# Kernel tuning notes

Hardware: AMD Instinct MI355X
Metric: run time of the kernel (lower is better)

The kernel has to match this reference:

```python
import jax, jax.numpy as jnp
import numpy as np

B, S, E = 2, 2048, 1024
H = 16
D = E // H
LAYER_IDX = 2.0
MASKED_BIAS = -10000.0


def setup_inputs() -> dict:
    key = jax.random.key(0)
    k1, k2, k3 = jax.random.split(key, 3)
    hidden_state = jax.random.normal(k1, (B, S, E), dtype=jnp.float32)
    w_attn = jax.random.normal(k2, (E, 3 * E), dtype=jnp.float32) * 0.2
    b_attn = jnp.zeros((3 * E,), dtype=jnp.float32)
    w_proj = jax.random.normal(k3, (E, E), dtype=jnp.float32) * 0.2
    b_proj = jnp.zeros((E,), dtype=jnp.float32)
    return {"hidden_state": hidden_state, "w_attn": w_attn, "b_attn": b_attn,
            "w_proj": w_proj, "b_proj": b_proj}


def reference(hidden_state, w_attn, b_attn, w_proj, b_proj):
    b, s, e = hidden_state.shape
    # c_attn: Conv1D == x @ W + b, then split into q, k, v
    qkv = hidden_state @ w_attn + b_attn          # [b, s, 3E]
    q, k, v = jnp.split(qkv, 3, axis=-1)
    # split heads -> [b, H, s, D]
    def split_heads(t):
        return t.reshape(b, s, H, D).transpose(0, 2, 1, 3)
    q, k, v = split_heads(q), split_heads(k), split_heads(v)
    # QK^T scaled by sqrt(d_head) then by layer_idx
    scores = jnp.einsum("bhqd,bhkd->bhqk", q, k)
    scores = scores / jnp.asarray(D ** 0.5, scores.dtype)
    scores = scores / LAYER_IDX
    # causal mask with masked_bias fill (-10000.0), matching bias buffer slice
    causal = jnp.tril(jnp.ones((s, s), dtype=bool))  # [s, s]
    scores = jnp.where(causal[None, None, :, :], scores, jnp.asarray(MASKED_BIAS, scores.dtype))
    attn = jax.nn.softmax(scores, axis=-1)
    out = jnp.einsum("bhqk,bhkd->bhqd", attn, v)   # [b, H, s, D]
    # merge heads
    out = out.transpose(0, 2, 1, 3).reshape(b, s, e)
    # c_proj
    return out @ w_proj + b_proj
```

## Files before the change

kernel.cpp:

```cpp
#include <hip/hip_runtime.h>
#include <cstddef>
#include <cstdint>

#define B_DIM   2
#define S_LEN   2048
#define EMB     1024
#define NH      16
#define HD      64
#define QKV_N   3072
#define MROWS   (B_DIM * S_LEN)

using half8  = __attribute__((ext_vector_type(8))) _Float16;
using half4  = __attribute__((ext_vector_type(4))) _Float16;
using f32x4  = __attribute__((ext_vector_type(4))) float;

#if defined(__has_builtin)
#if __has_builtin(__builtin_amdgcn_global_load_lds)
#define HAS_GLL 1
#endif
#endif

__device__ __forceinline__ void stage16(const _Float16* g, _Float16* lds_base, int lane)
{
#ifdef HAS_GLL
    (void)lane;
    __builtin_amdgcn_global_load_lds(
        (const __attribute__((address_space(1))) unsigned int*)g,
        (__attribute__((address_space(3))) unsigned int*)lds_base, 16, 0, 0);
#else
    *(half8*)(lds_base + lane * 8) = *(const half8*)g;
#endif
}

__global__ __launch_bounds__(256)
void prep_all(const float* __restrict__ hidden, const float* __restrict__ w_attn,
              const float* __restrict__ w_proj, _Float16* __restrict__ hidden_h,
              _Float16* __restrict__ wattn_t, _Float16* __restrict__ wproj_t)
{
    const int bid = blockIdx.x, t = threadIdx.x;
    if (bid < 4096) {
        int i = bid * 1024 + t * 4;
        float4 v = *(const float4*)(hidden + i);
        half4 h = { (_Float16)v.x, (_Float16)v.y, (_Float16)v.z, (_Float16)v.w };
        *(half4*)(hidden_h + i) = h;
        return;
    }
    __shared__ float T[32][33];
    const float* W; _Float16* Wt; int N, bx, by;
    if (bid < 7168) {
        int t2 = bid - 4096; bx = t2 % 96; by = t2 / 96; W = w_attn; Wt = wattn_t; N = QKV_N;
    } else {
        int t3 = bid - 7168; bx = t3 & 31; by = t3 >> 5; W = w_proj; Wt = wproj_t; N = EMB;
    }
    const int n0 = bx * 32, k0 = by * 32;
    const int r = t >> 3, c4 = (t & 7) * 4;
    float4 w = *(const float4*)(W + (size_t)(k0 + r) * N + n0 + c4);
    T[r][c4 + 0] = w.x; T[r][c4 + 1] = w.y;
    T[r][c4 + 2] = w.z; T[r][c4 + 3] = w.w;
    __syncthreads();
    half4 h = { (_Float16)T[c4 + 0][r], (_Float16)T[c4 + 1][r],
                (_Float16)T[c4 + 2][r], (_Float16)T[c4 + 3][r] };
    *(half4*)(Wt + (size_t)(n0 + r) * EMB + k0 + c4) = h;
}

template <int MT, int MINW, bool OUT_F16, bool FUSE_VT>
__global__ __launch_bounds__(256, MINW)
void hgemm_lds(const _Float16* __restrict__ X, const _Float16* __restrict__ Wt,
               const float* __restrict__ bias, void* __restrict__ Cout,
               _Float16* __restrict__ vt, int M, int N, int K)
{
    constexpr int BM = MT * 32;
    constexpr int ACALLS = BM / 32;
    __shared__ _Float16 As[BM][64];
    __shared__ _Float16 Bs[128][64];

    const int tid  = threadIdx.x;
    const int wave = tid >> 6, lane = tid & 63;
    const int quad = lane >> 4, l15 = lane & 15;
    const int wm = (wave >> 1) * (MT * 16);
    const int wn = (wave & 1) * 64;
    const int m0 = blockIdx.y * BM, n0 = blockIdx.x * 128;

    const int srow = lane >> 3;
    const int scol = ((lane & 7) ^ srow) * 8;

    const _Float16* xg[ACALLS];
#pragma unroll
    for (int c = 0; c < ACALLS; ++c)
        xg[c] = X + (size_t)(m0 + wave * (BM / 4) + c * 8 + srow) * K + scol;
    const _Float16* wg[4];
#pragma unroll
    for (int c = 0; c < 4; ++c)
        wg[c] = Wt + (size_t)(n0 + wave * 32 + c * 8 + srow) * K + scol;

    f32x4 acc[MT][4] = {};
    const int sx = l15 & 7;

    for (int k0 = 0; k0 < K; k0 += 64) {
#pragma unroll
        for (int c = 0; c < ACALLS; ++c)
            stage16(xg[c] + k0, &As[wave * (BM / 4) + c * 8][0], lane);
#pragma unroll
        for (int c = 0; c < 4; ++c)
            stage16(wg[c] + k0, &Bs[wave * 32 + c * 8][0], lane);
        __syncthreads();

#pragma unroll
        for (int cc = 0; cc < 2; ++cc) {
            half8 af[MT], bf[4];
#pragma unroll
            for (int mt = 0; mt < MT; ++mt)
                af[mt] = *(const half8*)&As[wm + mt * 16 + l15][(((cc * 4 + quad) ^ sx)) * 8];
#pragma unroll
            for (int nt = 0; nt < 4; ++nt)
                bf[nt] = *(const half8*)&Bs[wn + nt * 16 + l15][(((cc * 4 + quad) ^ sx)) * 8];
#pragma unroll
            for (int mt = 0; mt < MT; ++mt)
#pragma unroll
                for (int nt = 0; nt < 4; ++nt)
                    acc[mt][nt] = __builtin_amdgcn_mfma_f32_16x16x32_f16(
                        af[mt], bf[nt], acc[mt][nt], 0, 0, 0);
        }
        __syncthreads();
    }

    if (FUSE_VT && n0 >= 2 * EMB) {
#pragma unroll
        for (int nt = 0; nt < 4; ++nt) {
            const int c  = n0 + wn + nt * 16 + l15;
            const float bv = bias[c];
            const int vcol = c - 2 * EMB;
            const int hh = vcol >> 6, dd = vcol & 63;
#pragma unroll
            for (int mt = 0; mt < MT; ++mt) {
                const int r = m0 + wm + mt * 16 + quad * 4;
                const int bb = r >> 11, ss = r & 2047;
                half4 o = { (_Float16)(acc[mt][nt][0] + bv), (_Float16)(acc[mt][nt][1] + bv),
                            (_Float16)(acc[mt][nt][2] + bv), (_Float16)(acc[mt][nt][3] + bv) };
                *(half4*)(vt + ((size_t)(bb * NH + hh) * HD + dd) * S_LEN + ss) = o;
            }
        }
        return;
    }

#pragma unroll
    for (int nt = 0; nt < 4; ++nt) {
        const int c = n0 + wn + nt * 16 + l15;
        const float bv = bias[c];
#pragma unroll
        for (int mt = 0; mt < MT; ++mt)
#pragma unroll
            for (int reg = 0; reg < 4; ++reg) {
                const int r = m0 + wm + mt * 16 + quad * 4 + reg;
                const float v = acc[mt][nt][reg] + bv;
                if (OUT_F16)
                    ((_Float16*)Cout)[(size_t)r * N + c] = (_Float16)v;
                else
                    ((float*)Cout)[(size_t)r * N + c] = v;
            }
    }
}

__global__ __launch_bounds__(256, 2)
void attn_fa_mfma7(const _Float16* __restrict__ qkv,
                   const _Float16* __restrict__ vt,
                   _Float16* __restrict__ outh)
{
    __shared__ _Float16 Ks[128][64];
    __shared__ _Float16 Vs[64][128];

    const int n   = blockIdx.x;
    const int xcd = n & 7, g = (n >> 3) & 3, j = n >> 5;
    const int bh  = xcd * 4 + g;
    const int qta = j, qtb = 31 - j;
    const int b = bh >> 4, h = bh & 15;

    const int tid  = threadIdx.x;
    const int wave = tid >> 6, lane = tid & 63;
    const int quad = lane >> 4, l15 = lane & 15;
    const size_t row0 = (size_t)b * S_LEN;

    const _Float16 qscale = (_Float16)0.0901684400555602f;
    half8 qfa[2], qfb[2];
    {
        const _Float16* qpa = qkv + (row0 + qta * 64 + wave * 16 + l15) * QKV_N + h * HD + quad * 8;
        const _Float16* qpb = qkv + (row0 + qtb * 64 + wave * 16 + l15) * QKV_N + h * HD + quad * 8;
#pragma unroll
        for (int c = 0; c < 2; ++c) {
            half8 qa = *(const half8*)(qpa + c * 32);
            half8 qb = *(const half8*)(qpb + c * 32);
#pragma unroll
            for (int j2 = 0; j2 < 8; ++j2) { qa[j2] *= qscale; qb[j2] *= qscale; }
            qfa[c] = qa; qfb[c] = qb;
        }
    }

    f32x4 o_a[4] = {}, o_b[4] = {};
    float m_a = -1e30f, l_a = 0.0f, m_b = -1e30f, l_b = 0.0f;

    const int ksrow = lane >> 3;
    const int kscol = ((lane & 7) ^ ksrow) * 8;
    const int vsrow = lane >> 4;
    const _Float16* vbase = vt + (size_t)bh * HD * S_LEN;
    const int sxk = l15 & 7;

    auto softmax_pack = [&](f32x4 (&st)[8], half4 (&pf)[8], float& m_i, float& l_i,
                            f32x4 (&o_acc)[4]) {
        float rm = fmaxf(fmaxf(st[0][0], st[0][1]), fmaxf(st[0][2], st[0][3]));
#pragma unroll
        for (int nt = 1; nt < 8; ++nt) {
            rm = fmaxf(rm, fmaxf(st[nt][0], st[nt][1]));
            rm = fmaxf(rm, fmaxf(st[nt][2], st[nt][3]));
        }
        rm = fmaxf(rm, __shfl_xor(rm, 16));
        rm = fmaxf(rm, __shfl_xor(rm, 32));
        const float mnew = fmaxf(m_i, rm);
        if (__ballot(mnew > m_i)) {
            const float alpha = __builtin_amdgcn_exp2f(m_i - mnew);
            l_i *= alpha;
#pragma unroll
            for (int dt = 0; dt < 4; ++dt)
#pragma unroll
                for (int reg = 0; reg < 4; ++reg) o_acc[dt][reg] *= alpha;
        }
        m_i = mnew;
        float rs = 0.0f;
#pragma unroll
        for (int nt = 0; nt < 8; ++nt) {
            float p0 = __builtin_amdgcn_exp2f(st[nt][0] - mnew);
            float p1 = __builtin_amdgcn_exp2f(st[nt][1] - mnew);
            float p2 = __builtin_amdgcn_exp2f(st[nt][2] - mnew);
            float p3 = __builtin_amdgcn_exp2f(st[nt][3] - mnew);
            rs += (p0 + p1) + (p2 + p3);
            pf[nt] = half4{ (_Float16)p0, (_Float16)p1, (_Float16)p2, (_Float16)p3 };
        }
        rs += __shfl_xor(rs, 16);
        rs += __shfl_xor(rs, 32);
        l_i += rs;
    };

    const int ktNa = (qta + 2) >> 1;
    const int ktNb = (qtb + 2) >> 1;

    for (int kt = 0; kt < ktNb; ++kt) {
        __syncthreads();
        {
            const _Float16* kbase = qkv + (row0 + kt * 128) * QKV_N + EMB + h * HD;
#pragma unroll
            for (int c = 0; c < 4; ++c) {
                const int r0 = wave * 32 + c * 8;
                stage16(kbase + (size_t)(r0 + ksrow) * QKV_N + kscol, &Ks[r0][0], lane);
            }
#pragma unroll
            for (int c = 0; c < 4; ++c) {
                const int r0 = wave * 16 + c * 4;
                const int sgv = ((lane & 15) ^ (c * 4 + vsrow)) * 8;
                stage16(vbase + (size_t)(r0 + vsrow) * S_LEN + kt * 128 + sgv, &Vs[r0][0], lane);
            }
        }
        __syncthreads();

        if (kt < ktNa) {
            f32x4 sa[8] = {}, sb[8] = {};
#pragma unroll
            for (int c = 0; c < 2; ++c)
#pragma unroll
                for (int nt = 0; nt < 8; ++nt) {
                    half8 kf = *(const half8*)&Ks[nt * 16 + l15][((c * 4 + quad) ^ sxk) * 8];
                    sa[nt] = __builtin_amdgcn_mfma_f32_16x16x32_f16(kf, qfa[c], sa[nt], 0, 0, 0);
                    sb[nt] = __builtin_amdgcn_mfma_f32_16x16x32_f16(kf, qfb[c], sb[nt], 0, 0, 0);
                }
            if (kt == ktNa - 1) {
                const int q = qta * 64 + wave * 16 + l15;
#pragma unroll
                for (int nt = 0; nt < 8; ++nt) {
                    const int ks = kt * 128 + nt * 16 + quad * 4;
#pragma unroll
                    for (int reg = 0; reg < 4; ++reg)
                        if (ks + reg > q) sa[nt][reg] = -1e30f;
                }
            }
            half4 pfa[8], pfb[8];
            softmax_pack(sa, pfa, m_a, l_a, o_a);
            softmax_pack(sb, pfb, m_b, l_b, o_b);
#pragma unroll
            for (int nt = 0; nt < 8; ++nt)
#pragma unroll
                for (int dt = 0; dt < 4; ++dt) {
                    const int pg = ((2 * nt + (quad >> 1)) ^ l15) * 8 + (quad & 1) * 4;
                    half4 vf = *(const half4*)&Vs[dt * 16 + l15][pg];
                    o_a[dt] = __builtin_amdgcn_mfma_f32_16x16x16f16(vf, pfa[nt], o_a[dt], 0, 0, 0);
                    o_b[dt] = __builtin_amdgcn_mfma_f32_16x16x16f16(vf, pfb[nt], o_b[dt], 0, 0, 0);
                }
        } else {
            f32x4 sb[8] = {};
#pragma unroll
            for (int c = 0; c < 2; ++c)
#pragma unroll
                for (int nt = 0; nt < 8; ++nt) {
                    half8 kf = *(const half8*)&Ks[nt * 16 + l15][((c * 4 + quad) ^ sxk) * 8];
                    sb[nt] = __builtin_amdgcn_mfma_f32_16x16x32_f16(kf, qfb[c], sb[nt], 0, 0, 0);
                }
            if (kt == ktNb - 1) {
                const int q = qtb * 64 + wave * 16 + l15;
#pragma unroll
                for (int nt = 0; nt < 8; ++nt) {
                    const int ks = kt * 128 + nt * 16 + quad * 4;
#pragma unroll
                    for (int reg = 0; reg < 4; ++reg)
                        if (ks + reg > q) sb[nt][reg] = -1e30f;
                }
            }
            half4 pfb[8];
            softmax_pack(sb, pfb, m_b, l_b, o_b);
#pragma unroll
            for (int nt = 0; nt < 8; ++nt)
#pragma unroll
                for (int dt = 0; dt < 4; ++dt) {
                    const int pg = ((2 * nt + (quad >> 1)) ^ l15) * 8 + (quad & 1) * 4;
                    half4 vf = *(const half4*)&Vs[dt * 16 + l15][pg];
                    o_b[dt] = __builtin_amdgcn_mfma_f32_16x16x16f16(vf, pfb[nt], o_b[dt], 0, 0, 0);
                }
        }
    }

    {
        const float inv = 1.0f / l_a;
        const size_t r = row0 + qta * 64 + wave * 16 + l15;
#pragma unroll
        for (int dt = 0; dt < 4; ++dt) {
            half4 o = { (_Float16)(o_a[dt][0] * inv), (_Float16)(o_a[dt][1] * inv),
                        (_Float16)(o_a[dt][2] * inv), (_Float16)(o_a[dt][3] * inv) };
            *(half4*)(outh + r * EMB + h * HD + dt * 16 + quad * 4) = o;
        }
    }
    {
        const float inv = 1.0f / l_b;
        const size_t r = row0 + qtb * 64 + wave * 16 + l15;
#pragma unroll
        for (int dt = 0; dt < 4; ++dt) {
            half4 o = { (_Float16)(o_b[dt][0] * inv), (_Float16)(o_b[dt][1] * inv),
                        (_Float16)(o_b[dt][2] * inv), (_Float16)(o_b[dt][3] * inv) };
            *(half4*)(outh + r * EMB + h * HD + dt * 16 + quad * 4) = o;
        }
    }
}

extern "C" void kernel_launch(void* const* d_in, const int* in_sizes, int n_in,
                              void* d_out, int out_size, void* d_ws, size_t ws_size,
                              hipStream_t stream)
{
    const float* hidden = (const float*)d_in[0];
    const float* w_attn = (const float*)d_in[1];
    const float* b_attn = (const float*)d_in[2];
    const float* w_proj = (const float*)d_in[3];
    const float* b_proj = (const float*)d_in[4];

    _Float16* hidden_h = (_Float16*)d_ws;
    _Float16* wattn_t  = hidden_h + (size_t)MROWS * EMB;
    _Float16* wproj_t  = wattn_t + (size_t)EMB * QKV_N;
    _Float16* qkv_h    = wproj_t + (size_t)EMB * EMB;
    _Float16* attn_h   = qkv_h + (size_t)MROWS * QKV_N;
    _Float16* vt       = attn_h + (size_t)MROWS * EMB;

    prep_all<<<8192, 256, 0, stream>>>(hidden, w_attn, w_proj,
                                       hidden_h, wattn_t, wproj_t);

    hgemm_lds<4, 3, true, true><<<dim3(QKV_N / 128, MROWS / 128), 256, 0, stream>>>(
        hidden_h, wattn_t, b_attn, qkv_h, vt, MROWS, QKV_N, EMB);

    attn_fa_mfma7<<<dim3(512), 256, 0, stream>>>(qkv_h, vt, attn_h);

    hgemm_lds<2, 4, false, false><<<dim3(EMB / 128, MROWS / 64), 256, 0, stream>>>(
        attn_h, wproj_t, b_proj, d_out, nullptr, MROWS, EMB, EMB);
}
```

Baseline: 170.3 us.

## Read K and V fragments directly from global memory in attention kernel

The attention kernel no longer stages K and V tiles into shared memory with swizzled layouts and block barriers. Each wave now loads its MFMA operand fragments straight from global memory (K rows from the qkv buffer, V from the transposed buffer). This removes LDS traffic and both __syncthreads per key tile. In exchange, all four waves redundantly fetch the same K/V data through the caches, and the strided global loads (row stride 3072 halves for K) may be poorly coalesced and add latency.

```diff
diff --git a/kernel.cpp b/kernel.cpp
--- a/kernel.cpp
+++ b/kernel.cpp
@@ -162,13 +162,10 @@
 }
 
 __global__ __launch_bounds__(256, 2)
-void attn_fa_mfma7(const _Float16* __restrict__ qkv,
-                   const _Float16* __restrict__ vt,
-                   _Float16* __restrict__ outh)
-{
-    __shared__ _Float16 Ks[128][64];
-    __shared__ _Float16 Vs[64][128];
-
+void attn_fa_mfma11(const _Float16* __restrict__ qkv,
+                    const _Float16* __restrict__ vt,
+                    _Float16* __restrict__ outh)
+{
     const int n   = blockIdx.x;
     const int xcd = n & 7, g = (n >> 3) & 3, j = n >> 5;
     const int bh  = xcd * 4 + g;
@@ -198,11 +195,7 @@
     f32x4 o_a[4] = {}, o_b[4] = {};
     float m_a = -1e30f, l_a = 0.0f, m_b = -1e30f, l_b = 0.0f;
 
-    const int ksrow = lane >> 3;
-    const int kscol = ((lane & 7) ^ ksrow) * 8;
-    const int vsrow = lane >> 4;
     const _Float16* vbase = vt + (size_t)bh * HD * S_LEN;
-    const int sxk = l15 & 7;
 
     auto softmax_pack = [&](f32x4 (&st)[8], half4 (&pf)[8], float& m_i, float& l_i,
                             f32x4 (&o_acc)[4]) {
@@ -243,22 +236,8 @@
     const int ktNb = (qtb + 2) >> 1;
 
     for (int kt = 0; kt < ktNb; ++kt) {
-        __syncthreads();
-        {
-            const _Float16* kbase = qkv + (row0 + kt * 128) * QKV_N + EMB + h * HD;
-#pragma unroll
-            for (int c = 0; c < 4; ++c) {
-                const int r0 = wave * 32 + c * 8;
-                stage16(kbase + (size_t)(r0 + ksrow) * QKV_N + kscol, &Ks[r0][0], lane);
-            }
-#pragma unroll
-            for (int c = 0; c < 4; ++c) {
-                const int r0 = wave * 16 + c * 4;
-                const int sgv = ((lane & 15) ^ (c * 4 + vsrow)) * 8;
-                stage16(vbase + (size_t)(r0 + vsrow) * S_LEN + kt * 128 + sgv, &Vs[r0][0], lane);
-            }
-        }
-        __syncthreads();
+        const _Float16* kb = qkv + (row0 + kt * 128) * QKV_N + EMB + h * HD;
+        const _Float16* vb = vbase + kt * 128;
 
         if (kt < ktNa) {
             f32x4 sa[8] = {}, sb[8] = {};
@@ -266,7 +245,7 @@
             for (int c = 0; c < 2; ++c)
 #pragma unroll
                 for (int nt = 0; nt < 8; ++nt) {
-                    half8 kf = *(const half8*)&Ks[nt * 16 + l15][((c * 4 + quad) ^ sxk) * 8];
+                    half8 kf = *(const half8*)(kb + (size_t)(nt * 16 + l15) * QKV_N + c * 32 + quad * 8);
                     sa[nt] = __builtin_amdgcn_mfma_f32_16x16x32_f16(kf, qfa[c], sa[nt], 0, 0, 0);
                     sb[nt] = __builtin_amdgcn_mfma_f32_16x16x32_f16(kf, qfb[c], sb[nt], 0, 0, 0);
                 }
@@ -287,8 +266,8 @@
             for (int nt = 0; nt < 8; ++nt)
 #pragma unroll
                 for (int dt = 0; dt < 4; ++dt) {
-                    const int pg = ((2 * nt + (quad >> 1)) ^ l15) * 8 + (quad & 1) * 4;
-                    half4 vf = *(const half4*)&Vs[dt * 16 + l15][pg];
+                    half4 vf = *(const half4*)(vb + (size_t)(dt * 16 + l15) * S_LEN
+                                               + (2 * nt + (quad >> 1)) * 8 + (quad & 1) * 4);
                     o_a[dt] = __builtin_amdgcn_mfma_f32_16x16x16f16(vf, pfa[nt], o_a[dt], 0, 0, 0);
                     o_b[dt] = __builtin_amdgcn_mfma_f32_16x16x16f16(vf, pfb[nt], o_b[dt], 0, 0, 0);
                 }
@@ -298,7 +277,7 @@
             for (int c = 0; c < 2; ++c)
 #pragma unroll
                 for (int nt = 0; nt < 8; ++nt) {
-                    half8 kf = *(const half8*)&Ks[nt * 16 + l15][((c * 4 + quad) ^ sxk) * 8];
+                    half8 kf = *(const half8*)(kb + (size_t)(nt * 16 + l15) * QKV_N + c * 32 + quad * 8);
                     sb[nt] = __builtin_amdgcn_mfma_f32_16x16x32_f16(kf, qfb[c], sb[nt], 0, 0, 0);
                 }
             if (kt == ktNb - 1) {
@@ -317,8 +296,8 @@
             for (int nt = 0; nt < 8; ++nt)
 #pragma unroll
                 for (int dt = 0; dt < 4; ++dt) {
-                    const int pg = ((2 * nt + (quad >> 1)) ^ l15) * 8 + (quad & 1) * 4;
-                    half4 vf = *(const half4*)&Vs[dt * 16 + l15][pg];
+                    half4 vf = *(const half4*)(vb + (size_t)(dt * 16 + l15) * S_LEN
+                                               + (2 * nt + (quad >> 1)) * 8 + (quad & 1) * 4);
                     o_b[dt] = __builtin_amdgcn_mfma_f32_16x16x16f16(vf, pfb[nt], o_b[dt], 0, 0, 0);
                 }
         }
@@ -369,7 +348,7 @@
     hgemm_lds<4, 3, true, true><<<dim3(QKV_N / 128, MROWS / 128), 256, 0, stream>>>(
         hidden_h, wattn_t, b_attn, qkv_h, vt, MROWS, QKV_N, EMB);
 
-    attn_fa_mfma7<<<dim3(512), 256, 0, stream>>>(qkv_h, vt, attn_h);
+    attn_fa_mfma11<<<dim3(512), 256, 0, stream>>>(qkv_h, vt, attn_h);
 
     hgemm_lds<2, 4, false, false><<<dim3(EMB / 128, MROWS / 64), 256, 0, stream>>>(
         attn_h, wproj_t, b_proj, d_out, nullptr, MROWS, EMB, EMB);
```

Result: slower. 289.9 us (+70.2%).
